# Optimization experiments

Hardware: AMD Instinct MI355X
Metric: run time of the kernel (lower is better)

Reference implementation:

```python
import jax, jax.numpy as jnp
import numpy as np

NB_FEATURES = 128
ACCUMULATION = 4


def iterative_inv(mat, n_iter=6):
    # Newton-Schulz iteration for matrix inverse ('original' init: global max)
    I = jnp.eye(mat.shape[-1], dtype=mat.dtype)
    K = mat
    V = (1.0 / jnp.max(jnp.sum(K, axis=-2))) * jnp.swapaxes(K, -1, -2)
    for _ in range(n_iter):
        KV = K @ V
        V = 0.25 * V @ (13.0 * I - KV @ (15.0 * I - KV @ (7.0 * I - KV)))
    return V


def setup_inputs() -> dict:
    key = jax.random.key(0)
    kq, kk, kv, ks = jax.random.split(key, 4)
    b, h, n, d = 4, 8, 2048, 64
    q = jax.random.normal(kq, (b, h, n, d), dtype=jnp.float32)
    k = jax.random.normal(kk, (b, h, n, d), dtype=jnp.float32)
    v = jax.random.normal(kv, (b, h, n, d), dtype=jnp.float32)
    mask = jnp.ones((b, n), dtype=jnp.float32)
    total = ACCUMULATION * NB_FEATURES
    # uniform_sketching: indices in [0,n) scaled by non_padding_num (=n here),
    # second half of the flat index list offset by +n to index the k-block of X.
    S = jax.random.randint(ks, (b, total), 0, n)
    S = S.at[:, total // 2:].add(n)
    sketching_matrix = S.reshape(b, ACCUMULATION, NB_FEATURES)
    random_sign = jnp.ones((b, ACCUMULATION, NB_FEATURES), dtype=jnp.float32)
    return {"q": q, "k": k, "v": v, "mask": mask,
            "random_sign": random_sign, "sketching_matrix": sketching_matrix}


def reference(q, k, v, mask, random_sign, sketching_matrix):
    b, h, n, d = q.shape
    data_normalizer = 32.0 ** (-0.25)
    m = mask[:, None, :, None]                      # [b,1,n,1]
    q = q * (m * data_normalizer)
    k = k * (m * data_normalizer)
    v = v * m

    X = jnp.concatenate([q, k], axis=2)             # [b,h,2n,d]
    Xt = jnp.transpose(X, (0, 2, 1, 3))             # [b,2n,h,d]
    XS = Xt[jnp.arange(b)[:, None, None], sketching_matrix]  # [b,acc,f,h,d]
    XS = jnp.transpose(XS, (0, 3, 1, 2, 4))         # [b,h,acc,f,d]

    # RS-RBF kernel sketch: exp(x.y - |x|^2/2 - |y|^2/2), accumulated over acc
    diag1 = (0.5 * jnp.sum(X * X, axis=-1))[:, :, None, :, None]   # [b,h,1,2n,1]
    diag2 = (0.5 * jnp.sum(XS * XS, axis=-1))[:, :, :, None, :]    # [b,h,acc,1,f]
    prod = jnp.einsum('bhnp,bhmfp->bhmnf', X, XS) - diag1 - diag2  # [b,h,acc,2n,f]
    res = jnp.exp(prod)
    res = jnp.transpose(res, (0, 1, 3, 2, 4))       # [b,h,2n,acc,f]
    AS = jnp.einsum('bhnmf,bmf->bhnf', res, random_sign)  # [b,h,2n,f]

    Q = AS[:, :, :n]                                # [b,h,n,f]
    K = AS[:, :, n:]                                # [b,h,n,f]

    ASt = jnp.transpose(AS, (0, 2, 1, 3))           # [b,2n,h,f]
    STAS = ASt[jnp.arange(b)[:, None, None], sketching_matrix]     # [b,acc,f,h,f]
    STAS = jnp.einsum('bmdhe,bmd->bhde', STAS, random_sign)        # [b,h,f,f]
    f = STAS.shape[-1]
    STAS = STAS + 0.1 * jnp.eye(f, dtype=STAS.dtype)

    D_inv = jnp.sqrt(1.0 / jnp.sum(STAS, axis=-1))  # [b,h,f]
    STAS_n = D_inv[..., :, None] * STAS * D_inv[..., None, :]
    STAS_inv = iterative_inv(STAS_n, 6)

    K = (K * D_inv[:, :, None, :]) @ STAS_inv       # [b,h,n,f]
    K = K * D_inv[:, :, None, :] * m

    context = jnp.einsum('bhnf,bhne->bhfe', K, v)   # [b,h,f,d]
    out = Q @ context                               # [b,h,n,d]
    return out
```

## Files before the change

### kernel.cpp

```cpp
#include <hip/hip_runtime.h>

constexpr int Bc = 4, Hc = 8, Nc = 2048, Dc = 64, Fc = 128, Mc = 4;
constexpr int BHc = Bc*Hc;
constexpr int T2c = 2*Nc;
constexpr int Jc  = Mc*Fc;
constexpr float DNORM = 0.4204482076268573f;

constexpr size_t OFF_AS    = 0;
constexpr size_t OFF_XSH   = OFF_AS    + (size_t)BHc*T2c*Fc;
constexpr size_t OFF_XSM   = OFF_XSH   + (size_t)BHc*Jc*Dc/2;
constexpr size_t OFF_XSL   = OFF_XSM   + (size_t)BHc*Jc*Dc/2;
constexpr size_t OFF_DIAG1 = OFF_XSL   + (size_t)BHc*Jc*Dc/2;
constexpr size_t OFF_DIAG2 = OFF_DIAG1 + (size_t)BHc*T2c;
constexpr size_t OFF_STASN = OFF_DIAG2 + (size_t)BHc*Jc;
constexpr size_t OFF_VBUF  = OFF_STASN + (size_t)BHc*Fc*Fc;
constexpr size_t OFF_DINV  = OFF_VBUF  + (size_t)BHc*Fc*Fc;
constexpr size_t OFF_GMAX  = OFF_DINV  + (size_t)BHc*Fc;
constexpr size_t OFF_CTX   = OFF_GMAX  + 64;
constexpr size_t OFF_KH    = OFF_CTX   + (size_t)BHc*Fc*Dc;
constexpr size_t OFF_KM    = OFF_KH    + (size_t)BHc*Fc*Fc/2;
constexpr size_t OFF_KL    = OFF_KM    + (size_t)BHc*Fc*Fc/2;
constexpr size_t OFF_GPART = OFF_XSH;
constexpr size_t OFF_ZSC   = OFF_GPART + (size_t)BHc*4*128*64;

typedef __attribute__((ext_vector_type(8))) short bf16x8;
typedef __attribute__((ext_vector_type(4))) float f32x4;
typedef __attribute__((ext_vector_type(4))) unsigned short u16x4;

__device__ __forceinline__ unsigned short f2bf_rne(float x) {
  unsigned int u = __float_as_uint(x);
  u += 0x7fff + ((u >> 16) & 1);
  return (unsigned short)(u >> 16);
}
__device__ __forceinline__ float bf2f(unsigned short h) {
  return __uint_as_float(((unsigned int)h) << 16);
}

__global__ __launch_bounds__(256) void diag1_kernel(
    const float* __restrict__ q, const float* __restrict__ k,
    const float* __restrict__ mask, float* __restrict__ diag1) {
  int gid = blockIdx.x*256 + threadIdx.x;
  int kq  = gid & 15;
  int row = gid >> 4;
  int t   = row & (T2c - 1);
  int bh  = row >> 12;
  int b   = bh >> 3;
  int tn  = (t < Nc) ? t : t - Nc;
  const float* src = ((t < Nc) ? q : k) + ((size_t)bh*Nc + tn)*Dc;
  float sc = DNORM * mask[b*Nc + tn];
  float4 x = *(const float4*)(src + kq*4);
  float s = x.x*x.x + x.y*x.y + x.z*x.z + x.w*x.w;
  s += __shfl_xor(s, 1);
  s += __shfl_xor(s, 2);
  s += __shfl_xor(s, 4);
  s += __shfl_xor(s, 8);
  if (kq == 0) diag1[row] = 0.5f * sc * sc * s;
}

__global__ __launch_bounds__(256) void gather_kernel(
    const float* __restrict__ q, const float* __restrict__ k,
    const float* __restrict__ mask, const int* __restrict__ sketch,
    const float* __restrict__ diag1,
    unsigned short* __restrict__ xsh, unsigned short* __restrict__ xsm,
    unsigned short* __restrict__ xsl, float* __restrict__ diag2) {
  int gid = blockIdx.x*256 + threadIdx.x;
  int kq  = gid & 15;
  int idx = gid >> 4;
  int j   = idx & (Jc - 1);
  int bh  = idx >> 9;
  int b   = bh >> 3;
  int t   = sketch[b*Jc + j];
  int tn  = (t < Nc) ? t : t - Nc;
  const float* src = ((t < Nc) ? q : k) + ((size_t)bh*Nc + tn)*Dc;
  float sc = DNORM * mask[b*Nc + tn];
  float4 x = *(const float4*)(src + kq*4);
  float xv[4] = {x.x*sc, x.y*sc, x.z*sc, x.w*sc};
  u16x4 hh, mm_, ll;
  #pragma unroll
  for (int jj = 0; jj < 4; ++jj) {
    unsigned short h = f2bf_rne(xv[jj]);
    float r1 = xv[jj] - bf2f(h);
    unsigned short m = f2bf_rne(r1);
    float r2 = r1 - bf2f(m);
    hh[jj] = h; mm_[jj] = m; ll[jj] = f2bf_rne(r2);
  }
  *(u16x4*)(xsh + (size_t)idx*Dc + kq*4) = hh;
  *(u16x4*)(xsm + (size_t)idx*Dc + kq*4) = mm_;
  *(u16x4*)(xsl + (size_t)idx*Dc + kq*4) = ll;
  if (kq == 0) diag2[idx] = diag1[bh*T2c + t];
}

__global__ __launch_bounds__(256) void as_mfma_kernel(
    const float* __restrict__ q, const float* __restrict__ k,
    const float* __restrict__ mask,
    const unsigned short* __restrict__ xsh, const unsigned short* __restrict__ xsm,
    const unsigned short* __restrict__ xsl,
    const float* __restrict__ diag1, const float* __restrict__ diag2,
    const float* __restrict__ sign, float* __restrict__ AS) {
  __shared__ __align__(16) unsigned short Ah[64][72];
  __shared__ __align__(16) unsigned short Am[64][72];
  __shared__ __align__(16) unsigned short Al[64][72];
  __shared__ float d1s[64];
  __shared__ float d2s[4][128];
  __shared__ float sgs[4][128];
  int bh = blockIdx.y, b = bh >> 3;
  int t0 = blockIdx.x * 64;
  int tid = threadIdx.x;
  int lane = tid & 63, wid = tid >> 6;
  int wr = wid >> 1, wc = wid & 1;
  int l16 = lane & 15, lg = lane >> 4;
  int R0 = wr*32, C0 = wc*64;

  for (int i = tid; i < 64*16; i += 256) {
    int r = i >> 4, kq = i & 15;
    int t = t0 + r;
    int tn = (t < Nc) ? t : t - Nc;
    const float* src = ((t < Nc) ? q : k) + ((size_t)bh*Nc + tn)*Dc + kq*4;
    float sc = DNORM * mask[b*Nc + tn];
    float4 x = *(const float4*)src;
    float xv[4] = {x.x*sc, x.y*sc, x.z*sc, x.w*sc};
    u16x4 hv, mv, lv;
    #pragma unroll
    for (int jj = 0; jj < 4; ++jj) {
      unsigned short h = f2bf_rne(xv[jj]);
      float r1 = xv[jj] - bf2f(h);
      unsigned short m = f2bf_rne(r1);
      float r2 = r1 - bf2f(m);
      hv[jj] = h; mv[jj] = m; lv[jj] = f2bf_rne(r2);
    }
    *(u16x4*)&Ah[r][kq*4] = hv;
    *(u16x4*)&Am[r][kq*4] = mv;
    *(u16x4*)&Al[r][kq*4] = lv;
  }
  if (tid < 64) d1s[tid] = diag1[bh*T2c + t0 + tid];
  for (int i = tid; i < 512; i += 256) {
    d2s[i>>7][i&127] = diag2[bh*Jc + i];
    sgs[i>>7][i&127] = sign[b*Jc + i];
  }
  __syncthreads();

  const unsigned short* xhh = xsh + (size_t)bh*Jc*Dc;
  const unsigned short* xmm = xsm + (size_t)bh*Jc*Dc;
  const unsigned short* xll = xsl + (size_t)bh*Jc*Dc;
  f32x4 oa[2][4];
  #pragma unroll
  for (int m = 0; m < 2; ++m)
    #pragma unroll
    for (int n = 0; n < 4; ++n) oa[m][n] = 0.f;

  for (int m = 0; m < Mc; ++m) {
    f32x4 acc[2][4];
    #pragma unroll
    for (int mm = 0; mm < 2; ++mm)
      #pragma unroll
      for (int nn = 0; nn < 4; ++nn) acc[mm][nn] = 0.f;
    #pragma unroll
    for (int kc = 0; kc < Dc; kc += 32) {
      int ko = kc + lg*8;
      bf16x8 ah[2], am2[2], al2[2], bhv[4], bmv[4], blv[4];
      #pragma unroll
      for (int mm = 0; mm < 2; ++mm) {
        ah[mm]  = *(const bf16x8*)&Ah[R0+16*mm+l16][ko];
        am2[mm] = *(const bf16x8*)&Am[R0+16*mm+l16][ko];
        al2[mm] = *(const bf16x8*)&Al[R0+16*mm+l16][ko];
      }
      #pragma unroll
      for (int nn = 0; nn < 4; ++nn) {
        size_t p = (size_t)(m*Fc + C0 + 16*nn + l16)*Dc + ko;
        bhv[nn] = *(const bf16x8*)(xhh + p);
        bmv[nn] = *(const bf16x8*)(xmm + p);
        blv[nn] = *(const bf16x8*)(xll + p);
      }
      #pragma unroll
      for (int mm = 0; mm < 2; ++mm)
        #pragma unroll
        for (int nn = 0; nn < 4; ++nn) {
          acc[mm][nn] = __builtin_amdgcn_mfma_f32_16x16x32_bf16(am2[mm], bmv[nn], acc[mm][nn], 0,0,0);
          acc[mm][nn] = __builtin_amdgcn_mfma_f32_16x16x32_bf16(ah[mm],  blv[nn], acc[mm][nn], 0,0,0);
          acc[mm][nn] = __builtin_amdgcn_mfma_f32_16x16x32_bf16(al2[mm], bhv[nn], acc[mm][nn], 0,0,0);
          acc[mm][nn] = __builtin_amdgcn_mfma_f32_16x16x32_bf16(ah[mm],  bmv[nn], acc[mm][nn], 0,0,0);
          acc[mm][nn] = __builtin_amdgcn_mfma_f32_16x16x32_bf16(am2[mm], bhv[nn], acc[mm][nn], 0,0,0);
          acc[mm][nn] = __builtin_amdgcn_mfma_f32_16x16x32_bf16(ah[mm],  bhv[nn], acc[mm][nn], 0,0,0);
        }
    }
    #pragma unroll
    for (int mm = 0; mm < 2; ++mm)
      #pragma unroll
      for (int nn = 0; nn < 4; ++nn) {
        int c = C0 + 16*nn + l16;
        float d2v = d2s[m][c], sg = sgs[m][c];
        #pragma unroll
        for (int r = 0; r < 4; ++r) {
          int row = R0 + 16*mm + 4*lg + r;
          oa[mm][nn][r] += sg * __expf(acc[mm][nn][r] - d1s[row] - d2v);
        }
      }
  }
  #pragma unroll
  for (int mm = 0; mm < 2; ++mm)
    #pragma unroll
    for (int nn = 0; nn < 4; ++nn) {
      int c = C0 + 16*nn + l16;
      #pragma unroll
      for (int r = 0; r < 4; ++r) {
        int row = R0 + 16*mm + 4*lg + r;
        AS[((size_t)bh*T2c + t0 + row)*Fc + c] = oa[mm][nn][r];
      }
    }
}

__global__ __launch_bounds__(256) void stas_kernel(
    const float* __restrict__ AS, const int* __restrict__ sketch,
    const float* __restrict__ sign,
    float* __restrict__ STASn, float* __restrict__ Dinv,
    unsigned short* __restrict__ Kh, unsigned short* __restrict__ Km,
    unsigned short* __restrict__ Kl,
    unsigned int* __restrict__ gmax) {
  extern __shared__ float stas[];
  __shared__ int   Ssh[Jc];
  __shared__ float sgn[Jc];
  __shared__ float Dl[Fc];
  __shared__ float red[Fc];
  int bh = blockIdx.x;
  int b  = bh >> 3;
  int tid = threadIdx.x;
  for (int i = tid; i < Jc; i += 256) {
    Ssh[i] = sketch[b*Jc + i];
    sgn[i] = sign[b*Jc + i];
  }
  __syncthreads();
  for (int i = tid; i < Fc*Fc; i += 256) {
    int dd = i >> 7, e = i & 127;
    float vsum = 0.f;
    #pragma unroll
    for (int m = 0; m < Mc; ++m) {
      int t = Ssh[m*Fc + dd];
      vsum += sgn[m*Fc + dd] * AS[((size_t)bh*T2c + t)*Fc + e];
    }
    if (dd == e) vsum += 0.1f;
    stas[dd*129 + e] = vsum;
  }
  __syncthreads();
  if (tid < Fc) {
    float s = 0.f;
    for (int e = 0; e < Fc; ++e) s += stas[tid*129 + e];
    float di = 1.0f / sqrtf(s);
    Dl[tid] = di;
    Dinv[bh*Fc + tid] = di;
  }
  __syncthreads();
  for (int i = tid; i < Fc*Fc; i += 256) {
    int dd = i >> 7, e = i & 127;
    float vv = stas[dd*129 + e] * Dl[dd] * Dl[e];
    stas[dd*129 + e] = vv;
    STASn[(size_t)bh*Fc*Fc + i] = vv;
    unsigned short hb = f2bf_rne(vv); float r1 = vv - bf2f(hb);
    unsigned short mb = f2bf_rne(r1); float r2 = r1 - bf2f(mb);
    Kh[(size_t)bh*Fc*Fc + i] = hb;
    Km[(size_t)bh*Fc*Fc + i] = mb;
    Kl[(size_t)bh*Fc*Fc + i] = f2bf_rne(r2);
  }
  __syncthreads();
  if (tid < Fc) {
    float s = 0.f;
    for (int dd = 0; dd < Fc; ++dd) s += stas[dd*129 + tid];
    red[tid] = s;
  }
  __syncthreads();
  if (tid == 0) {
    float mx = 0.f;
    for (int e = 0; e < Fc; ++e) mx = fmaxf(mx, red[e]);
    atomicMax(gmax, __float_as_uint(mx));
  }
}

__device__ __forceinline__ unsigned boff(int brow, int ke) {
  unsigned byte = ((unsigned)brow << 8) | ((unsigned)ke << 1);
  return byte ^ (((unsigned)(brow & 7)) << 4);
}

__device__ __forceinline__ void mm6(const bf16x8 ah[2], const bf16x8 am[2], const bf16x8 al[2],
                                    const bf16x8 bh[4], const bf16x8 bm[4], const bf16x8 bl[4],
                                    f32x4 acc[2][4]) {
  #pragma unroll
  for (int m = 0; m < 2; ++m)
    #pragma unroll
    for (int n = 0; n < 4; ++n) {
      acc[m][n] = __builtin_amdgcn_mfma_f32_16x16x32_bf16(am[m], bm[n], acc[m][n], 0,0,0);
      acc[m][n] = __builtin_amdgcn_mfma_f32_16x16x32_bf16(ah[m], bl[n], acc[m][n], 0,0,0);
      acc[m][n] = __builtin_amdgcn_mfma_f32_16x16x32_bf16(al[m], bh[n], acc[m][n], 0,0,0);
      acc[m][n] = __builtin_amdgcn_mfma_f32_16x16x32_bf16(ah[m], bm[n], acc[m][n], 0,0,0);
      acc[m][n] = __builtin_amdgcn_mfma_f32_16x16x32_bf16(am[m], bh[n], acc[m][n], 0,0,0);
      acc[m][n] = __builtin_amdgcn_mfma_f32_16x16x32_bf16(ah[m], bh[n], acc[m][n], 0,0,0);
    }
}

__device__ __forceinline__ void ld3(const char* Ph, const char* Pm, const char* Pl,
                                    int brow, int ko, bf16x8& h, bf16x8& m, bf16x8& l) {
  unsigned off = boff(brow, ko);
  h = *(const bf16x8*)(Ph + off);
  m = *(const bf16x8*)(Pm + off);
  l = *(const bf16x8*)(Pl + off);
}

__device__ __forceinline__ void mm_p1(
    const unsigned short* __restrict__ kh, const unsigned short* __restrict__ km,
    const unsigned short* __restrict__ kl,
    const char* Ah, const char* Am, const char* Al,
    int R0, int C0, int l16, int lg, f32x4 acc[2][4]) {
  #pragma unroll 1
  for (int kc = 0; kc < Fc; kc += 32) {
    int ko = kc + lg*8;
    bf16x8 ah[2], am[2], al[2], bh[4], bm[4], bl[4];
    #pragma unroll
    for (int m = 0; m < 2; ++m) {
      size_t p = (size_t)(R0+16*m+l16)*Fc + ko;
      ah[m] = *(const bf16x8*)(kh + p);
      am[m] = *(const bf16x8*)(km + p);
      al[m] = *(const bf16x8*)(kl + p);
    }
    #pragma unroll
    for (int n = 0; n < 4; ++n)
      ld3(Ah, Am, Al, C0+16*n+l16, ko, bh[n], bm[n], bl[n]);
    mm6(ah, am, al, bh, bm, bl, acc);
  }
}

__device__ __forceinline__ void mm_p234(
    const char* Ah, const char* Am, const char* Al,
    const char* Zh, const char* Zm, const unsigned short* __restrict__ ZlG,
    int R0, int C0, int l16, int lg, f32x4 acc[2][4]) {
  #pragma unroll 1
  for (int kc = 0; kc < Fc; kc += 32) {
    int ko = kc + lg*8;
    bf16x8 ah[2], am[2], al[2], bh[4], bm[4], bl[4];
    #pragma unroll
    for (int m = 0; m < 2; ++m)
      ld3(Ah, Am, Al, R0+16*m+l16, ko, ah[m], am[m], al[m]);
    #pragma unroll
    for (int n = 0; n < 4; ++n) {
      int col = C0+16*n+l16;
      unsigned off = boff(col, ko);
      bh[n] = *(const bf16x8*)(Zh + off);
      bm[n] = *(const bf16x8*)(Zm + off);
      bl[n] = *(const bf16x8*)(ZlG + col*Fc + ko);
    }
    mm6(ah, am, al, bh, bm, bl, acc);
  }
}

__device__ __forceinline__ void split4(f32x4 v, u16x4& hv, u16x4& mv, u16x4& lv) {
  #pragma unroll
  for (int r = 0; r < 4; ++r) {
    unsigned short hb = f2bf_rne(v[r]); float r1 = v[r] - bf2f(hb);
    unsigned short mb = f2bf_rne(r1);   float r2 = r1 - bf2f(mb);
    hv[r] = hb; mv[r] = mb; lv[r] = f2bf_rne(r2);
  }
}
__device__ __forceinline__ void wbA3(char* Ah, char* Am, char* Al,
                                     int col, int row0, f32x4 v) {
  u16x4 hv, mv, lv;
  split4(v, hv, mv, lv);
  unsigned off = boff(col, row0);
  *(u16x4*)(Ah + off) = hv;
  *(u16x4*)(Am + off) = mv;
  *(u16x4*)(Al + off) = lv;
}
__device__ __forceinline__ void wbZ3(char* Zh, char* Zm, unsigned short* __restrict__ ZlG,
                                     int col, int row0, f32x4 v) {
  u16x4 hv, mv, lv;
  split4(v, hv, mv, lv);
  unsigned off = boff(col, row0);
  *(u16x4*)(Zh + off) = hv;
  *(u16x4*)(Zm + off) = mv;
  *(u16x4*)(ZlG + col*Fc + row0) = lv;
}

__global__ __launch_bounds__(512) void newton_ctx_kernel(
    const float* __restrict__ STASn,
    const unsigned short* __restrict__ KhG, const unsigned short* __restrict__ KmG,
    const unsigned short* __restrict__ KlG,
    const float* __restrict__ gmaxf, float* __restrict__ Vout,
    const float* __restrict__ ASg, const float* __restrict__ vg,
    const float* __restrict__ maskg, float* __restrict__ Gpart,
    unsigned short* __restrict__ ZlScr) {
  extern __shared__ char smc[];
  int tid  = threadIdx.x;

  if (blockIdx.x < BHc) {
    char* Ah = smc;
    char* Am = smc + 32768;
    char* Al = smc + 65536;
    char* Zh = smc + 98304;
    char* Zm = smc + 131072;
    int bh = blockIdx.x;
    const float* Kp = STASn + (size_t)bh*Fc*Fc;
    const unsigned short* kh = KhG + (size_t)bh*Fc*Fc;
    const unsigned short* km = KmG + (size_t)bh*Fc*Fc;
    const unsigned short* kl = KlG + (size_t)bh*Fc*Fc;
    unsigned short* ZlG = ZlScr + (size_t)bh*Fc*Fc;
    float ginv = 1.0f / gmaxf[0];
    int lane = tid & 63;
    int wid  = tid >> 6;
    int wr = wid >> 1, wc = wid & 1;
    int l16 = lane & 15, lg = lane >> 4;
    int R0 = wr*32, C0 = wc*64;
    int drow0 = lg*4;

    f32x4 vreg[2][4];
    #pragma unroll
    for (int m = 0; m < 2; ++m)
      #pragma unroll
      for (int n = 0; n < 4; ++n) {
        int col = C0 + 16*n + l16;
        #pragma unroll
        for (int r = 0; r < 4; ++r)
          vreg[m][n][r] = Kp[(size_t)(R0 + 16*m + drow0 + r)*Fc + col] * ginv;
        wbA3(Ah, Am, Al, col, R0 + 16*m + drow0, vreg[m][n]);
      }
    __syncthreads();

    f32x4 fin[2][4];
    for (int it = 0; it < 6; ++it) {
      f32x4 acc[2][4];
      #pragma unroll
      for (int m = 0; m < 2; ++m) for (int n = 0; n < 4; ++n) acc[m][n] = 0.f;
      mm_p1(kh, km, kl, Ah, Am, Al, R0, C0, l16, lg, acc);
      #pragma unroll
      for (int m = 0; m < 2; ++m)
        #pragma unroll
        for (int n = 0; n < 4; ++n)
          wbZ3(Zh, Zm, ZlG, C0 + 16*n + l16, R0 + 16*m + drow0, acc[m][n]);
      __syncthreads();

      #pragma unroll
      for (int m = 0; m < 2; ++m) for (int n = 0; n < 4; ++n) acc[m][n] = 0.f;
      mm_p234(Ah, Am, Al, Zh, Zm, ZlG, R0, C0, l16, lg, acc);
      #pragma unroll
      for (int m = 0; m < 2; ++m)
        #pragma unroll
        for (int n = 0; n < 4; ++n)
          fin[m][n] = 13.f*vreg[m][n] - 15.f*acc[m][n];
      __syncthreads();
      #pragma unroll
      for (int m = 0; m < 2; ++m)
        #pragma unroll
        for (int n = 0; n < 4; ++n)
          wbA3(Ah, Am, Al, C0 + 16*n + l16, R0 + 16*m + drow0, acc[m][n]);
      __syncthreads();

      #pragma unroll
      for (int m = 0; m < 2; ++m) for (int n = 0; n < 4; ++n) acc[m][n] = 0.f;
      mm_p234(Ah, Am, Al, Zh, Zm, ZlG, R0, C0, l16, lg, acc);
      #pragma unroll
      for (int m = 0; m < 2; ++m)
        #pragma unroll
        for (int n = 0; n < 4; ++n)
          fin[m][n] += 7.f*acc[m][n];
      __syncthreads();
      #pragma unroll
      for (int m = 0; m < 2; ++m)
        #pragma unroll
        for (int n = 0; n < 4; ++n)
          wbA3(Ah, Am, Al, C0 + 16*n + l16, R0 + 16*m + drow0, acc[m][n]);
      __syncthreads();

      #pragma unroll
      for (int m = 0; m < 2; ++m) for (int n = 0; n < 4; ++n) acc[m][n] = 0.f;
      mm_p234(Ah, Am, Al, Zh, Zm, ZlG, R0, C0, l16, lg, acc);
      #pragma unroll
      for (int m = 0; m < 2; ++m)
        #pragma unroll
        for (int n = 0; n < 4; ++n) {
          fin[m][n] = 0.25f*(fin[m][n] - acc[m][n]);
          vreg[m][n] = fin[m][n];
        }
      __syncthreads();
      #pragma unroll
      for (int m = 0; m < 2; ++m)
        #pragma unroll
        for (int n = 0; n < 4; ++n)
          wbA3(Ah, Am, Al, C0 + 16*n + l16, R0 + 16*m + drow0, fin[m][n]);
      __syncthreads();
    }

    float* Vo = Vout + (size_t)bh*Fc*Fc;
    #pragma unroll
    for (int m = 0; m < 2; ++m)
      #pragma unroll
      for (int n = 0; n < 4; ++n) {
        int col = C0 + 16*n + l16;
        #pragma unroll
        for (int r = 0; r < 4; ++r)
          Vo[(size_t)(R0 + 16*m + drow0 + r)*Fc + col] = vreg[m][n][r];
      }
  } else {
    float* Ksh = (float*)smc;
    float* vsh = (float*)(smc + 32768);
    int id = blockIdx.x - BHc;
    int cbh = id >> 2, chunk = id & 3;
    int cb = cbh >> 3;
    int t0 = chunk * 512;
    int f = tid & 127, g = tid >> 7;
    float acc[16];
    #pragma unroll
    for (int j = 0; j < 16; ++j) acc[j] = 0.f;
    for (int sub = 0; sub < 8; ++sub) {
      __syncthreads();
      int ts = t0 + sub*64;
      for (int i = tid; i < 64*32; i += 512) {
        int r = i >> 5, c4 = i & 31;
        *(float4*)&Ksh[r*128 + c4*4] =
            *(const float4*)(ASg + ((size_t)cbh*T2c + Nc + ts + r)*Fc + c4*4);
      }
      for (int i = tid; i < 64*16; i += 512) {
        int r = i >> 4, c4 = i & 15;
        float mk = maskg[cb*Nc + ts + r];
        float m2 = mk*mk;
        float4 x = *(const float4*)(vg + ((size_t)cbh*Nc + ts + r)*Dc + c4*4);
        x.x*=m2; x.y*=m2; x.z*=m2; x.w*=m2;
        *(float4*)&vsh[r*64 + c4*4] = x;
      }
      __syncthreads();
      #pragma unroll 2
      for (int tl = 0; tl < 64; ++tl) {
        float kf = Ksh[tl*128 + f];
        #pragma unroll
        for (int j4 = 0; j4 < 4; ++j4) {
          float4 vv = *(const float4*)&vsh[tl*64 + g*16 + j4*4];
          acc[j4*4+0] += kf*vv.x; acc[j4*4+1] += kf*vv.y;
          acc[j4*4+2] += kf*vv.z; acc[j4*4+3] += kf*vv.w;
        }
      }
    }
    float* gp = Gpart + ((((size_t)cbh*4 + chunk)*128 + f)*64 + g*16);
    #pragma unroll
    for (int j4 = 0; j4 < 4; ++j4)
      *(float4*)(gp + j4*4) = *(const float4*)&acc[j4*4];
  }
}

__global__ __launch_bounds__(256) void ctx_fix_kernel(
    const float* __restrict__ Gpart, const float* __restrict__ Vinv,
    const float* __restrict__ Dinv, float* __restrict__ ctxo) {
  __shared__ float DG[128*64];
  __shared__ float Dl[128];
  int bh = blockIdx.x;
  int tid = threadIdx.x;
  if (tid < 128) Dl[tid] = Dinv[bh*Fc + tid];
  __syncthreads();
  for (int i = tid; i < 2048; i += 256) {
    int e = i >> 4, c4 = i & 15;
    const float* g0 = Gpart + ((((size_t)bh*4)*128 + e)*64 + c4*4);
    float4 s0 = *(const float4*)(g0);
    float4 s1 = *(const float4*)(g0 + 8192);
    float4 s2 = *(const float4*)(g0 + 16384);
    float4 s3 = *(const float4*)(g0 + 24576);
    float de = Dl[e];
    float4 o;
    o.x = (s0.x+s1.x+s2.x+s3.x)*de;
    o.y = (s0.y+s1.y+s2.y+s3.y)*de;
    o.z = (s0.z+s1.z+s2.z+s3.z)*de;
    o.w = (s0.w+s1.w+s2.w+s3.w)*de;
    *(float4*)&DG[e*64 + c4*4] = o;
  }
  __syncthreads();
  int f = tid & 127, half = tid >> 7;
  float acc[32];
  #pragma unroll
  for (int j = 0; j < 32; ++j) acc[j] = 0.f;
  for (int e = 0; e < 128; ++e) {
    float s = Vinv[(size_t)bh*Fc*Fc + (size_t)e*Fc + f];
    #pragma unroll
    for (int j4 = 0; j4 < 8; ++j4) {
      float4 dg = *(const float4*)&DG[e*64 + half*32 + j4*4];
      acc[j4*4+0] += s*dg.x; acc[j4*4+1] += s*dg.y;
      acc[j4*4+2] += s*dg.z; acc[j4*4+3] += s*dg.w;
    }
  }
  float df = Dl[f];
  float* op = ctxo + (size_t)bh*Fc*Dc + f*Dc + half*32;
  #pragma unroll
  for (int j4 = 0; j4 < 8; ++j4) {
    float4 o;
    o.x = acc[j4*4+0]*df; o.y = acc[j4*4+1]*df;
    o.z = acc[j4*4+2]*df; o.w = acc[j4*4+3]*df;
    *(float4*)(op + j4*4) = o;
  }
}

__global__ __launch_bounds__(256) void out_kernel(
    const float* __restrict__ AS, const float* __restrict__ ctx,
    float* __restrict__ out) {
  extern __shared__ float smo[];
  float* Asq = smo;
  float* Cs  = smo + 64*132;
  int bh = blockIdx.y;
  int row0 = blockIdx.x * 64;
  int tid = threadIdx.x;
  int tr = tid >> 4, tc = tid & 15;
  for (int i = tid; i < 64*32; i += 256) {
    int r = i >> 5, kq = i & 31;
    *(float4*)&Asq[r*132 + kq*4] =
        *(const float4*)(AS + ((size_t)bh*T2c + row0 + r)*Fc + kq*4);
  }
  for (int i = tid; i < 128*16; i += 256) {
    int r = i >> 4, kq = i & 15;
    *(float4*)&Cs[r*64 + kq*4] =
        *(const float4*)(ctx + (size_t)bh*Fc*Dc + r*Dc + kq*4);
  }
  __syncthreads();
  float acc[4][4] = {};
  #pragma unroll 2
  for (int kk = 0; kk < Fc; ++kk) {
    float4 bv = *(const float4*)&Cs[kk*64 + tc*4];
    float a0 = Asq[(tr*4+0)*132 + kk];
    float a1 = Asq[(tr*4+1)*132 + kk];
    float a2 = Asq[(tr*4+2)*132 + kk];
    float a3 = Asq[(tr*4+3)*132 + kk];
    acc[0][0] += a0*bv.x; acc[0][1] += a0*bv.y; acc[0][2] += a0*bv.z; acc[0][3] += a0*bv.w;
    acc[1][0] += a1*bv.x; acc[1][1] += a1*bv.y; acc[1][2] += a1*bv.z; acc[1][3] += a1*bv.w;
    acc[2][0] += a2*bv.x; acc[2][1] += a2*bv.y; acc[2][2] += a2*bv.z; acc[2][3] += a2*bv.w;
    acc[3][0] += a3*bv.x; acc[3][1] += a3*bv.y; acc[3][2] += a3*bv.z; acc[3][3] += a3*bv.w;
  }
  #pragma unroll
  for (int i = 0; i < 4; ++i) {
    float4 o;
    o.x = acc[i][0]; o.y = acc[i][1]; o.z = acc[i][2]; o.w = acc[i][3];
    *(float4*)(out + ((size_t)bh*Nc + row0 + tr*4 + i)*Dc + tc*4) = o;
  }
}

extern "C" void kernel_launch(void* const* d_in, const int* in_sizes, int n_in,
                              void* d_out, int out_size, void* d_ws, size_t ws_size,
                              hipStream_t stream) {
  const float* q    = (const float*)d_in[0];
  const float* k    = (const float*)d_in[1];
  const float* v    = (const float*)d_in[2];
  const float* mask = (const float*)d_in[3];
  const float* sign = (const float*)d_in[4];
  const int*   sketch = (const int*)d_in[5];
  float* out = (float*)d_out;
  float* ws  = (float*)d_ws;

  unsigned short* xsh = (unsigned short*)(ws + OFF_XSH);
  unsigned short* xsm = (unsigned short*)(ws + OFF_XSM);
  unsigned short* xsl = (unsigned short*)(ws + OFF_XSL);
  unsigned short* kh  = (unsigned short*)(ws + OFF_KH);
  unsigned short* km  = (unsigned short*)(ws + OFF_KM);
  unsigned short* kl  = (unsigned short*)(ws + OFF_KL);
  unsigned short* zsc = (unsigned short*)(ws + OFF_ZSC);

  hipMemsetAsync(ws + OFF_GMAX, 0, sizeof(float), stream);

  diag1_kernel<<<BHc*T2c*16/256, 256, 0, stream>>>(q, k, mask, ws + OFF_DIAG1);
  gather_kernel<<<BHc*Jc*16/256, 256, 0, stream>>>(q, k, mask, sketch, ws + OFF_DIAG1,
                                                   xsh, xsm, xsl, ws + OFF_DIAG2);
  as_mfma_kernel<<<dim3(T2c/64, BHc), 256, 0, stream>>>(q, k, mask, xsh, xsm, xsl,
      ws + OFF_DIAG1, ws + OFF_DIAG2, sign, ws + OFF_AS);
  stas_kernel<<<BHc, 256, 128*129*sizeof(float), stream>>>(ws + OFF_AS, sketch, sign,
      ws + OFF_STASN, ws + OFF_DINV, kh, km, kl, (unsigned int*)(ws + OFF_GMAX));
  newton_ctx_kernel<<<BHc + 128, 512, 163840, stream>>>(ws + OFF_STASN, kh, km, kl,
      ws + OFF_GMAX, ws + OFF_VBUF, ws + OFF_AS, v, mask, ws + OFF_GPART, zsc);
  ctx_fix_kernel<<<BHc, 256, 0, stream>>>(ws + OFF_GPART, ws + OFF_VBUF,
      ws + OFF_DINV, ws + OFF_CTX);
  out_kernel<<<dim3(Nc/64, BHc), 256, (64*132 + 128*64)*sizeof(float), stream>>>(
      ws + OFF_AS, ws + OFF_CTX, out);
}
```

Before: 359.6 us.

## Stage sketch B-operand in swizzled LDS and double AS tile rows

The AS MFMA kernel now processes 128 rows per block with 512 threads. For each accumulation slice it cooperatively copies the hi/mid/lo bf16 sketch tiles into XOR-swizzled shared memory, so they are read from LDS rather than from global memory per wave. The A tiles use the same swizzle to avoid bank conflicts. This adds about 100KB of dynamic LDS and extra barriers per slice, which limits occupancy. A separate loop in mm_p1 is changed from unroll 1 to unroll 2.

```diff
diff --git a/kernel.cpp b/kernel.cpp
--- a/kernel.cpp
+++ b/kernel.cpp
@@ -90,28 +90,37 @@
   if (kq == 0) diag2[idx] = diag1[bh*T2c + t];
 }
 
-__global__ __launch_bounds__(256) void as_mfma_kernel(
+__device__ __forceinline__ unsigned poff(int r, int ke) {
+  unsigned byte = ((unsigned)r << 7) | ((unsigned)ke << 1);
+  return byte ^ (((unsigned)(r & 7)) << 4);
+}
+
+__global__ __launch_bounds__(512) void as_mfma_kernel(
     const float* __restrict__ q, const float* __restrict__ k,
     const float* __restrict__ mask,
     const unsigned short* __restrict__ xsh, const unsigned short* __restrict__ xsm,
     const unsigned short* __restrict__ xsl,
     const float* __restrict__ diag1, const float* __restrict__ diag2,
     const float* __restrict__ sign, float* __restrict__ AS) {
-  __shared__ __align__(16) unsigned short Ah[64][72];
-  __shared__ __align__(16) unsigned short Am[64][72];
-  __shared__ __align__(16) unsigned short Al[64][72];
-  __shared__ float d1s[64];
-  __shared__ float d2s[4][128];
-  __shared__ float sgs[4][128];
+  extern __shared__ char sma[];
+  char* Ah = sma;
+  char* Am = sma + 16384;
+  char* Al = sma + 32768;
+  char* Bh = sma + 49152;
+  char* Bm = sma + 65536;
+  char* Bl = sma + 81920;
+  float* d1s = (float*)(sma + 98304);
+  float* d2s = (float*)(sma + 98816);
+  float* sgs = (float*)(sma + 100864);
   int bh = blockIdx.y, b = bh >> 3;
-  int t0 = blockIdx.x * 64;
+  int t0 = blockIdx.x * 128;
   int tid = threadIdx.x;
   int lane = tid & 63, wid = tid >> 6;
   int wr = wid >> 1, wc = wid & 1;
   int l16 = lane & 15, lg = lane >> 4;
   int R0 = wr*32, C0 = wc*64;
 
-  for (int i = tid; i < 64*16; i += 256) {
+  for (int i = tid; i < 128*16; i += 512) {
     int r = i >> 4, kq = i & 15;
     int t = t0 + r;
     int tn = (t < Nc) ? t : t - Nc;
@@ -128,16 +137,16 @@
       float r2 = r1 - bf2f(m);
       hv[jj] = h; mv[jj] = m; lv[jj] = f2bf_rne(r2);
     }
-    *(u16x4*)&Ah[r][kq*4] = hv;
-    *(u16x4*)&Am[r][kq*4] = mv;
-    *(u16x4*)&Al[r][kq*4] = lv;
-  }
-  if (tid < 64) d1s[tid] = diag1[bh*T2c + t0 + tid];
-  for (int i = tid; i < 512; i += 256) {
-    d2s[i>>7][i&127] = diag2[bh*Jc + i];
-    sgs[i>>7][i&127] = sign[b*Jc + i];
-  }
-  __syncthreads();
+    unsigned off = poff(r, kq*4);
+    *(u16x4*)(Ah + off) = hv;
+    *(u16x4*)(Am + off) = mv;
+    *(u16x4*)(Al + off) = lv;
+  }
+  if (tid < 128) d1s[tid] = diag1[bh*T2c + t0 + tid];
+  for (int i = tid; i < 512; i += 512) {
+    d2s[i] = diag2[bh*Jc + i];
+    sgs[i] = sign[b*Jc + i];
+  }
 
   const unsigned short* xhh = xsh + (size_t)bh*Jc*Dc;
   const unsigned short* xmm = xsm + (size_t)bh*Jc*Dc;
@@ -149,6 +158,17 @@
     for (int n = 0; n < 4; ++n) oa[m][n] = 0.f;
 
   for (int m = 0; m < Mc; ++m) {
+    __syncthreads();
+    for (int i = tid; i < 128*16; i += 512) {
+      int c = i >> 4, k4 = i & 15;
+      size_t p = (size_t)(m*Fc + c)*Dc + k4*4;
+      unsigned off = poff(c, k4*4);
+      *(u16x4*)(Bh + off) = *(const u16x4*)(xhh + p);
+      *(u16x4*)(Bm + off) = *(const u16x4*)(xmm + p);
+      *(u16x4*)(Bl + off) = *(const u16x4*)(xll + p);
+    }
+    __syncthreads();
+
     f32x4 acc[2][4];
     #pragma unroll
     for (int mm = 0; mm < 2; ++mm)
@@ -160,16 +180,17 @@
       bf16x8 ah[2], am2[2], al2[2], bhv[4], bmv[4], blv[4];
       #pragma unroll
       for (int mm = 0; mm < 2; ++mm) {
-        ah[mm]  = *(const bf16x8*)&Ah[R0+16*mm+l16][ko];
-        am2[mm] = *(const bf16x8*)&Am[R0+16*mm+l16][ko];
-        al2[mm] = *(const bf16x8*)&Al[R0+16*mm+l16][ko];
+        unsigned off = poff(R0+16*mm+l16, ko);
+        ah[mm]  = *(const bf16x8*)(Ah + off);
+        am2[mm] = *(const bf16x8*)(Am + off);
+        al2[mm] = *(const bf16x8*)(Al + off);
       }
       #pragma unroll
       for (int nn = 0; nn < 4; ++nn) {
-        size_t p = (size_t)(m*Fc + C0 + 16*nn + l16)*Dc + ko;
-        bhv[nn] = *(const bf16x8*)(xhh + p);
-        bmv[nn] = *(const bf16x8*)(xmm + p);
-        blv[nn] = *(const bf16x8*)(xll + p);
+        unsigned off = poff(C0+16*nn+l16, ko);
+        bhv[nn] = *(const bf16x8*)(Bh + off);
+        bmv[nn] = *(const bf16x8*)(Bm + off);
+        blv[nn] = *(const bf16x8*)(Bl + off);
       }
       #pragma unroll
       for (int mm = 0; mm < 2; ++mm)
@@ -188,7 +209,7 @@
       #pragma unroll
       for (int nn = 0; nn < 4; ++nn) {
         int c = C0 + 16*nn + l16;
-        float d2v = d2s[m][c], sg = sgs[m][c];
+        float d2v = d2s[m*Fc + c], sg = sgs[m*Fc + c];
         #pragma unroll
         for (int r = 0; r < 4; ++r) {
           int row = R0 + 16*mm + 4*lg + r;
@@ -308,7 +329,7 @@
     const unsigned short* __restrict__ kl,
     const char* Ah, const char* Am, const char* Al,
     int R0, int C0, int l16, int lg, f32x4 acc[2][4]) {
-  #pragma unroll 1
+  #pragma unroll 2
   for (int kc = 0; kc < Fc; kc += 32) {
     int ko = kc + lg*8;
     bf16x8 ah[2], am[2], al[2], bh[4], bm[4], bl[4];
@@ -656,7 +677,7 @@
   diag1_kernel<<<BHc*T2c*16/256, 256, 0, stream>>>(q, k, mask, ws + OFF_DIAG1);
   gather_kernel<<<BHc*Jc*16/256, 256, 0, stream>>>(q, k, mask, sketch, ws + OFF_DIAG1,
                                                    xsh, xsm, xsl, ws + OFF_DIAG2);
-  as_mfma_kernel<<<dim3(T2c/64, BHc), 256, 0, stream>>>(q, k, mask, xsh, xsm, xsl,
+  as_mfma_kernel<<<dim3(T2c/128, BHc), 512, 102912, stream>>>(q, k, mask, xsh, xsm, xsl,
       ws + OFF_DIAG1, ws + OFF_DIAG2, sign, ws + OFF_AS);
   stas_kernel<<<BHc, 256, 128*129*sizeof(float), stream>>>(ws + OFF_AS, sketch, sign,
       ws + OFF_STASN, ws + OFF_DINV, kh, km, kl, (unsigned int*)(ws + OFF_GMAX));
```

Result: faster. 331.6 us (-7.8%).
